# Kernel optimization log

Measured on AMD Instinct MI355X. Metric: run time of the kernel, lower is better.

## Reference

```python
import jax, jax.numpy as jnp
import numpy as np

H = 100      # STATE_SIZE
ATT = 100    # ATTENTION_SIZE
E = 32       # EMBEDDINGS_SIZE
V = 50257    # char vocab
TV = 60      # tag vocab
N = 2048     # source length (incl EOS padding)
T = 2048     # target length (incl EOS padding)
TT = 64      # number of tags


def lstm_cell(x, h, c, Wih, Whh, b):
    # torch gate order: i, f, g, o
    z = x @ Wih.T + h @ Whh.T + b
    i, f, g, o = jnp.split(z, 4)
    c = jax.nn.sigmoid(f) * c + jax.nn.sigmoid(i) * jnp.tanh(g)
    h = jax.nn.sigmoid(o) * jnp.tanh(c)
    return h, c


def lstm_scan(xs, Wih, Whh, b):
    Hs = Whh.shape[1]
    def step(carry, x):
        h, c = lstm_cell(x, carry[0], carry[1], Wih, Whh, b)
        return (h, c), h
    init = (jnp.zeros(Hs, xs.dtype), jnp.zeros(Hs, xs.dtype))
    _, ys = jax.lax.scan(step, init, xs)
    return ys


def setup_inputs() -> dict:
    key = jax.random.key(0)
    ks = iter(jax.random.split(key, 40))
    def rn(shape, s=0.1):
        return jax.random.normal(next(ks), shape, jnp.float32) * s
    return {
        "src_ids": jax.random.randint(next(ks), (1, N), 0, V),
        "tag_ids": jax.random.randint(next(ks), (1, TT), 0, TV),
        "out_ids": jax.random.randint(next(ks), (1, T), 0, V),
        "weight": jnp.ones((), jnp.float32),
        "emb_char": rn((V, E)),
        "emb_tag": rn((TV, E)),
        "enc_f_Wih": rn((4 * H, E)), "enc_f_Whh": rn((4 * H, H)), "enc_f_b": rn((4 * H,)),
        "enc_b_Wih": rn((4 * H, E)), "enc_b_Whh": rn((4 * H, H)), "enc_b_b": rn((4 * H,)),
        "tag_Wih": rn((4 * H, E)), "tag_Whh": rn((4 * H, H)), "tag_b": rn((4 * H,)),
        "dec_Wih": rn((4 * H, 3 * H + E)), "dec_Whh": rn((4 * H, H)), "dec_b": rn((4 * H,)),
        "attn_w1": rn((ATT, 2 * H)), "attn_w2": rn((ATT, 2 * H)), "attn_w3": rn((ATT, 5)),
        "attn_v": rn((1, ATT)),
        "tag_attn_w1": rn((ATT, H)), "tag_attn_w2": rn((ATT, 2 * H)), "tag_attn_v": rn((1, ATT)),
        "out_W": rn((V, H)), "out_b": rn((V,)),
    }


def reference(src_ids, tag_ids, out_ids, weight, emb_char, emb_tag,
              enc_f_Wih, enc_f_Whh, enc_f_b, enc_b_Wih, enc_b_Whh, enc_b_b,
              tag_Wih, tag_Whh, tag_b, dec_Wih, dec_Whh, dec_b,
              attn_w1, attn_w2, attn_w3, attn_v,
              tag_attn_w1, tag_attn_w2, tag_attn_v, out_W, out_b):
    x = emb_char[src_ids[0]]                       # (N, E)
    tg = emb_tag[tag_ids[0]]                       # (TT, E)
    # bidirectional char encoder
    yf = lstm_scan(x, enc_f_Wih, enc_f_Whh, enc_f_b)
    yb = lstm_scan(x[::-1], enc_b_Wih, enc_b_Whh, enc_b_b)[::-1]
    enc = jnp.concatenate([yf, yb], -1)            # (N, 2H)
    # tag encoder + self-attention residual (matches self_encode_tags)
    tv = lstm_scan(tg, tag_Wih, tag_Whh, tag_b)    # (TT, H)
    sa = jax.nn.softmax(tv @ tv.T, axis=-1)
    tagv = tv + jnp.einsum('sh,st->th', tv, sa)    # (TT, H)
    w1dt = enc @ attn_w1.T                         # (N, ATT)
    tag_w1dt = tagv @ tag_attn_w1.T                # (TT, ATT)
    eos_emb = emb_char[0]
    # initial decoder step on (enc_last, tag_last, eos_emb) with zero state
    x0 = jnp.concatenate([enc[-1], tagv[-1], eos_emb])
    h0, c0 = lstm_cell(x0, jnp.zeros(H, jnp.float32), jnp.zeros(H, jnp.float32),
                       dec_Wih, dec_Whh, dec_b)
    # teacher forcing: previous output embedding (EOS=id 0 at t=0)
    prev_ids = jnp.concatenate([jnp.zeros((1,), out_ids.dtype), out_ids[0, :-1]])
    prev_emb = emb_char[prev_ids]                  # (T, E)

    def step(carry, inp):
        h, c, prev_att = carry
        pe, oid = inp
        state = jnp.concatenate([h, c])            # (2H,)
        # tag attention
        taw = jax.nn.softmax(jnp.tanh(tag_w1dt + state @ tag_attn_w2.T) @ tag_attn_v[0])
        tag_ctx = taw @ tagv                       # (H,)
        new_state = state + jnp.concatenate([tag_ctx, tag_ctx])
        # char attention with 5-wide previous-attention feature
        scores = jnp.tanh(w1dt + new_state @ attn_w2.T + prev_att @ attn_w3.T) @ attn_v[0]
        aw = jax.nn.softmax(scores)                # (N,)
        ctx = aw @ enc                             # (2H,)
        startt = jnp.clip(jnp.argmax(aw) - 1, 0, N - 6)
        new_prev = jax.lax.dynamic_slice(aw, (startt,), (5,))
        hn, cn = lstm_cell(jnp.concatenate([ctx, tag_ctx, pe]), h, c,
                           dec_Wih, dec_Whh, dec_b)
        logits = hn @ out_W.T + out_b              # (V,)
        lt = -jax.nn.log_softmax(logits)[oid]
        return (hn, cn, new_prev), lt

    _, losses = jax.lax.scan(step, (h0, c0, jnp.zeros(5, jnp.float32)),
                             (prev_emb, out_ids[0]))
    return jnp.sum(losses) * weight
```

## Files before the change

kernel.cpp:

```cpp
#include <hip/hip_runtime.h>
#include <math.h>

#define NN   2048
#define TLEN 2048
#define TTAG 64
#define VOC  50257
#define GW   32
#define CHK  64
#define RECU 80
static_assert(GW * CHK == NN, "chunking");

#define OFF_XF    0
#define OFF_XB    (OFF_XF  + NN*400)
#define OFF_TGX   (OFF_XB  + NN*400)
#define OFF_PEW   (OFF_TGX + TTAG*400)
#define OFF_ENC   (OFF_PEW + TLEN*400)
#define OFF_W1DT  (OFF_ENC + NN*200)
#define OFF_TAGV  (OFF_W1DT+ NN*100)
#define OFF_TGW1  (OFF_TAGV+ TTAG*100)
#define OFF_TGW   (OFF_TGW1+ TTAG*100)
#define OFF_HOUT  (OFF_TGW + TTAG*400)
#define OFF_REC   (OFF_HOUT+ TLEN*100)
#define OFF_HC    (OFF_REC + 2*GW*RECU*2)
#define OFF_FLG   (OFF_HC  + 2*128*2)
#define OFF_PB    (OFF_FLG + 4096)


__device__ __forceinline__ float rcpf(float x){ return __builtin_amdgcn_rcpf(x); }
__device__ __forceinline__ float sigf(float x){ return rcpf(1.0f+__expf(-x)); }
__device__ __forceinline__ float tanhfast(float x){
  float e = __expf(2.0f*x);
  return 1.0f - 2.0f*rcpf(e+1.0f);
}
__device__ __forceinline__ unsigned short f2b(float x){
  unsigned b=__float_as_uint(x);
  return (unsigned short)((b + 0x7fffu + ((b>>16)&1u))>>16);
}
__device__ __forceinline__ unsigned pk2(float a,float b){ return (unsigned)f2b(a) | ((unsigned)f2b(b)<<16); }
__device__ __forceinline__ float blo(unsigned u){ return __uint_as_float(u<<16); }
__device__ __forceinline__ float bhi(unsigned u){ return __uint_as_float(u&0xffff0000u); }

__device__ __forceinline__ unsigned long long ald64(const unsigned long long* p){
  return __hip_atomic_load(p,__ATOMIC_RELAXED,__HIP_MEMORY_SCOPE_SYSTEM);
}
__device__ __forceinline__ void ast64(unsigned long long* p, unsigned long long v){
  __hip_atomic_store(p,v,__ATOMIC_RELAXED,__HIP_MEMORY_SCOPE_SYSTEM);
}
__device__ __forceinline__ void vm0(){ asm volatile("s_waitcnt vmcnt(0)" ::: "memory"); }

__global__ void kInit(float* ws){
  unsigned long long* f = (unsigned long long*)(ws + OFF_FLG);
  int i = blockIdx.x*256 + threadIdx.x;
  if (i < 2048) ast64(f+i, 0ull);
}

__global__ __launch_bounds__(512) void kPrep(
    const int* src, const int* tag, const int* oid,
    const float* emb_char, const float* emb_tag,
    const float* fWih, const float* fb,
    const float* bWih, const float* bb,
    const float* tWih, const float* tb,
    const float* dWih, const float* db, float* ws)
{
  int r = blockIdx.x, j = threadIdx.x;
  if (j >= 400) return;
  if (r < NN) {
    const float* e = emb_char + (size_t)src[r]*32;
    const float* Wr = fWih + j*32;
    float a = fb[j];
    #pragma unroll
    for (int q=0;q<32;q++) a += e[q]*Wr[q];
    ws[OFF_XF + r*400 + j] = a;
  } else if (r < 2*NN) {
    int n = r - NN;
    const float* e = emb_char + (size_t)src[n]*32;
    const float* Wr = bWih + j*32;
    float a = bb[j];
    #pragma unroll
    for (int q=0;q<32;q++) a += e[q]*Wr[q];
    ws[OFF_XB + n*400 + j] = a;
  } else if (r < 2*NN + TTAG) {
    int s = r - 2*NN;
    const float* e = emb_tag + (size_t)tag[s]*32;
    const float* Wr = tWih + j*32;
    float a = tb[j];
    #pragma unroll
    for (int q=0;q<32;q++) a += e[q]*Wr[q];
    ws[OFF_TGX + s*400 + j] = a;
  } else {
    int t = r - (2*NN + TTAG);
    int pid = (t==0) ? 0 : oid[t-1];
    const float* e = emb_char + (size_t)pid*32;
    const float* Wr = dWih + (size_t)j*332 + 300;
    float a = db[j];
    #pragma unroll
    for (int q=0;q<32;q++) a += e[q]*Wr[q];
    ws[OFF_PEW + t*400 + j] = a;
  }
}

struct EncShared {
  float tvs[TTAG*100];
  float sa [TTAG*64];
  float hbuf[100];
  float zbuf[400];
};

__device__ void lstm_block(const float* Whh, const float* xbase, float* ws,
                           int reverse, int col, EncShared* sh)
{
  int tid = threadIdx.x;
  float whh[100];
  if (tid < 400){
    #pragma unroll
    for (int k=0;k<100;k++) whh[k] = Whh[tid*100+k];
  }
  float c = 0.f;
  if (tid < 100) sh->hbuf[tid] = 0.f;
  __syncthreads();
  for (int i=0;i<NN;i++){
    int n = reverse ? (NN-1-i) : i;
    if (tid < 400){
      float z = xbase[n*400+tid];
      #pragma unroll
      for (int k=0;k<100;k++) z += whh[k]*sh->hbuf[k];
      sh->zbuf[tid] = z;
    }
    __syncthreads();
    if (tid < 100){
      float zi=sh->zbuf[tid], zf=sh->zbuf[tid+100], zg=sh->zbuf[tid+200], zo=sh->zbuf[tid+300];
      c = sigf(zf)*c + sigf(zi)*tanhfast(zg);
      float h = sigf(zo)*tanhfast(c);
      sh->hbuf[tid] = h;
      ws[OFF_ENC + n*200 + col + tid] = h;
    }
    __syncthreads();
  }
}

__global__ __launch_bounds__(512,1) void kEnc(
    const float* fWhh, const float* bWhh, const float* tWhh,
    const float* taw1, const float* dWih, float* ws)
{
  __shared__ EncShared sh;
  int b = blockIdx.x, tid = threadIdx.x;
  if (b == 0){ lstm_block(fWhh, ws+OFF_XF, ws, 0, 0,   &sh); return; }
  if (b == 1){ lstm_block(bWhh, ws+OFF_XB, ws, 1, 100, &sh); return; }

  {
    float whh[100];
    if (tid<400){
      #pragma unroll
      for (int k=0;k<100;k++) whh[k] = tWhh[tid*100+k];
    }
    float c = 0.f;
    if (tid<100) sh.hbuf[tid] = 0.f;
    __syncthreads();
    for (int s=0;s<TTAG;s++){
      if (tid<400){
        float z = ws[OFF_TGX + s*400 + tid];
        #pragma unroll
        for (int k=0;k<100;k++) z += whh[k]*sh.hbuf[k];
        sh.zbuf[tid] = z;
      }
      __syncthreads();
      if (tid<100){
        float zi=sh.zbuf[tid], zf=sh.zbuf[tid+100], zg=sh.zbuf[tid+200], zo=sh.zbuf[tid+300];
        c = sigf(zf)*c + sigf(zi)*tanhfast(zg);
        float h = sigf(zo)*tanhfast(c);
        sh.hbuf[tid] = h;
        sh.tvs[s*100+tid] = h;
      }
      __syncthreads();
    }
  }
  for (int idx=tid; idx<TTAG*TTAG; idx+=512){
    int s=idx>>6, t2=idx&63;
    float a=0.f;
    #pragma unroll 10
    for (int h=0;h<100;h++) a += sh.tvs[s*100+h]*sh.tvs[t2*100+h];
    sh.sa[idx]=a;
  }
  __syncthreads();
  if (tid<TTAG){
    float m=-1e30f;
    for (int t2=0;t2<64;t2++) m = fmaxf(m, sh.sa[tid*64+t2]);
    float sum=0.f;
    for (int t2=0;t2<64;t2++){ float e=__expf(sh.sa[tid*64+t2]-m); sh.sa[tid*64+t2]=e; sum+=e; }
    float r=1.f/sum;
    for (int t2=0;t2<64;t2++) sh.sa[tid*64+t2]*=r;
  }
  __syncthreads();
  float tvloc[13]; int cnt=0;
  for (int idx=tid; idx<TTAG*100; idx+=512){
    int t2=idx/100, hh=idx%100;
    float a = sh.tvs[t2*100+hh];
    for (int s=0;s<64;s++) a += sh.tvs[s*100+hh]*sh.sa[s*64+t2];
    tvloc[cnt++]=a;
    ws[OFF_TAGV+idx]=a;
  }
  __syncthreads();
  float* tagvs = sh.sa;
  cnt=0;
  for (int idx=tid; idx<TTAG*100; idx+=512) tagvs[idx]=tvloc[cnt++];
  __syncthreads();
  for (int idx=tid; idx<TTAG*100; idx+=512){
    int s=idx/100, k=idx%100;
    float a=0.f;
    #pragma unroll 10
    for (int h=0;h<100;h++) a += tagvs[s*100+h]*taw1[k*100+h];
    ws[OFF_TGW1+idx]=a;
  }
  for (int idx=tid; idx<TTAG*400; idx+=512){
    int s=idx/400, j=idx%400;
    const float* Wr = dWih + (size_t)j*332 + 200;
    float a=0.f;
    #pragma unroll 10
    for (int h=0;h<100;h++) a += tagvs[s*100+h]*Wr[h];
    ws[OFF_TGW+idx]=a;
  }
}

__global__ void kMid(const float* aw1, float* ws){
  __shared__ float er[200];
  int n=blockIdx.x, tid=threadIdx.x;
  for (int i=tid;i<200;i+=128) er[i]=ws[OFF_ENC+n*200+i];
  __syncthreads();
  if (tid<100){
    const float* Wr = aw1 + tid*200;
    float a=0.f;
    #pragma unroll 8
    for (int d=0;d<200;d++) a += er[d]*Wr[d];
    ws[OFF_W1DT + n*100 + tid]=a;
  }
}

__global__ __launch_bounds__(512) void kDec(
    const float* dWhh, const float* dWih,
    const float* aw2, const float* aw3, const float* av,
    const float* taw2, const float* tav, float* ws)
{
  __shared__ unsigned aw2L[100*101];
  __shared__ unsigned tw2L[100*101];
  __shared__ unsigned tw1L[TTAG*51];
  __shared__ unsigned tagvL[TTAG*51];
  __shared__ unsigned w1L[CHK*51];
  __shared__ unsigned encL[CHK*101];
  __shared__ float tavL[100], avL[100], aw3L[500];
  __shared__ float hL[100], cL[100], tcL[100], tsaL[100], nsL[200];
  __shared__ float uL[TTAG], tawL[TTAG];
  __shared__ float ctxL[200], a23L[100], ctxpL[200];
  __shared__ float srowL[CHK], eRL[CHK];
  __shared__ float zOwnL[16];
  __shared__ float prevL[5];
  __shared__ float Sg;
  __shared__ int   amiL;

  const int tid = threadIdx.x;
  const int w   = blockIdx.x;
  unsigned long long* REC = (unsigned long long*)(ws + OFF_REC);
  unsigned long long* HC  = (unsigned long long*)(ws + OFF_HC);
  unsigned long long* FLG = (unsigned long long*)(ws + OFF_FLG);

  const int nu = (w<4)? 4 : 3;
  const int u0 = (w<4)? w*4 : 16 + (w-4)*3;
  const int nact = nu*4;
  const int jslot = tid>>5, l = tid&31;

  unsigned wca0=0,wca1=0,wca2=0,wca3=0, wha0=0,wha1=0, wta0=0,wta1=0;
  int row=0;
  if (jslot < nact){
    row = (jslot&3)*100 + u0 + (jslot>>2);
    const float* Wr = dWih + (size_t)row*332;
    wca0=pk2(Wr[2*l],Wr[2*l+1]);
    wca1=pk2(Wr[2*(32+l)],Wr[2*(32+l)+1]);
    wca2=pk2(Wr[2*(64+l)],Wr[2*(64+l)+1]);
    if (l<4) wca3=pk2(Wr[2*(96+l)],Wr[2*(96+l)+1]);
    const float* Wh = dWhh + (size_t)row*100;
    wha0=pk2(Wh[2*l],Wh[2*l+1]);
    if (l<18) wha1=pk2(Wh[2*(32+l)],Wh[2*(32+l)+1]);
    const float* Wt = Wr + 200;
    wta0=pk2(Wt[2*l],Wt[2*l+1]);
    if (l<18) wta1=pk2(Wt[2*(32+l)],Wt[2*(32+l)+1]);
  }
  for (int i=tid;i<100*100;i+=512){ int k=i/100,p=i%100; aw2L[k*101+p]=pk2(aw2 [k*200+2*p], aw2 [k*200+2*p+1]); }
  for (int i=tid;i<100*100;i+=512){ int k=i/100,p=i%100; tw2L[k*101+p]=pk2(taw2[k*200+2*p], taw2[k*200+2*p+1]); }
  for (int i=tid;i<TTAG*50;i+=512){ int s=i/50,p=i%50; tw1L[s*51+p]=pk2(ws[OFF_TGW1+s*100+2*p], ws[OFF_TGW1+s*100+2*p+1]); }
  for (int i=tid;i<TTAG*50;i+=512){ int s=i/50,p=i%50; tagvL[s*51+p]=pk2(ws[OFF_TAGV+s*100+2*p], ws[OFF_TAGV+s*100+2*p+1]); }
  for (int i=tid;i<CHK*50;i+=512){ int r=i/50,p=i%50; w1L[r*51+p]=pk2(ws[OFF_W1DT+(w*CHK+r)*100+2*p], ws[OFF_W1DT+(w*CHK+r)*100+2*p+1]); }
  for (int i=tid;i<CHK*100;i+=512){ int r=i/100,p=i%100; encL[r*101+p]=pk2(ws[OFF_ENC+(w*CHK+r)*200+2*p], ws[OFF_ENC+(w*CHK+r)*200+2*p+1]); }
  if (tid<100){ tavL[tid]=tav[tid]; avL[tid]=av[tid]; }
  for (int i=tid;i<500;i+=512) aw3L[i]=aw3[i];
  if (tid<5)   prevL[tid]=0.f;
  if (tid<200) ctxL[tid]=ws[OFF_ENC + 2047*200 + tid];
  __syncthreads();

  if (jslot < nact){
    float acc=0.f;
    { unsigned u=wca0; acc += ctxL[2*l]*blo(u) + ctxL[2*l+1]*bhi(u); }
    { unsigned u=wca1; acc += ctxL[2*(32+l)]*blo(u) + ctxL[2*(32+l)+1]*bhi(u); }
    { unsigned u=wca2; acc += ctxL[2*(64+l)]*blo(u) + ctxL[2*(64+l)+1]*bhi(u); }
    if (l<4){ unsigned u=wca3; acc += ctxL[2*(96+l)]*blo(u) + ctxL[2*(96+l)+1]*bhi(u); }
    acc += __shfl_xor(acc,1,32); acc += __shfl_xor(acc,2,32);
    acc += __shfl_xor(acc,4,32); acc += __shfl_xor(acc,8,32); acc += __shfl_xor(acc,16,32);
    if (l==0) zOwnL[jslot] = acc + ws[OFF_TGW + 63*400 + row] + ws[OFF_PEW + row];
  }
  __syncthreads();
  float cOwn = 0.f;
  if (tid < nu){
    float zi=zOwnL[tid*4+0], zg=zOwnL[tid*4+2], zo=zOwnL[tid*4+3];
    float cc = sigf(zi)*tanhfast(zg);
    float hh = sigf(zo)*tanhfast(cc);
    cOwn = cc;
    ast64(HC + 128 + (u0+tid), (unsigned long long)pk2(hh,cc) | (1ull<<32));
  }

  for (int t=0; t<TLEN; ++t){
    const unsigned sq = (unsigned)(t+1);
    unsigned long long* slot = REC + (size_t)(t&1)*GW*RECU;
    unsigned long long* hcg  = HC + (size_t)((t+1)&1)*128;
    unsigned long long* hcp  = HC + (size_t)(t&1)*128;
    unsigned long long* fr   = FLG + (size_t)(t&1)*GW*16;
    unsigned long long* fh   = FLG + (size_t)(64 + (t&1)*GW)*16;

    if (tid < 100){
      const unsigned long long* p0 = hcg + tid;
      unsigned long long v;
      for(;;){ v=ald64(p0); if((unsigned)(v>>32)==sq) break; __builtin_amdgcn_s_sleep(1); }
      unsigned lo=(unsigned)v;
      hL[tid]=blo(lo); cL[tid]=bhi(lo);
    }
    __syncthreads();
    if (tid<400){
      int k=tid>>2, q=tid&3, off=q*50;
      const float* sb = (off<100)? (hL+off) : (cL+(off-100));
      float acc=0.f;
      #pragma unroll
      for (int i=0;i<25;i++){ unsigned u=tw2L[k*101+q*25+i]; acc += sb[2*i]*blo(u) + sb[2*i+1]*bhi(u); }
      acc += __shfl_xor(acc,1,4); acc += __shfl_xor(acc,2,4);
      if (q==0) tsaL[k]=acc;
    }
    __syncthreads();
    {
      int sp=tid>>3, l8=tid&7;
      float acc=0.f;
      for (int k=l8;k<100;k+=8){
        unsigned u=tw1L[sp*51+(k>>1)];
        float w1v=(k&1)? bhi(u) : blo(u);
        acc += tanhfast(w1v + tsaL[k]) * tavL[k];
      }
      acc += __shfl_xor(acc,1,8); acc += __shfl_xor(acc,2,8); acc += __shfl_xor(acc,4,8);
      if (l8==0) uL[sp]=acc;
    }
    __syncthreads();
    if (tid<64){
      float v=uL[tid], m=v;
      for (int d=1;d<64;d<<=1) m=fmaxf(m,__shfl_xor(m,d,64));
      float e=__expf(v-m), ssum=e;
      for (int d=1;d<64;d<<=1) ssum+=__shfl_xor(ssum,d,64);
      tawL[tid]=e*rcpf(ssum);
    }
    __syncthreads();
    if (tid<400){
      int hh=tid>>2, q=tid&3;
      float acc=0.f;
      #pragma unroll
      for (int i=0;i<16;i++){
        int s=q*16+i;
        unsigned u=tagvL[s*51+(hh>>1)];
        acc += tawL[s]*((hh&1)? bhi(u):blo(u));
      }
      acc += __shfl_xor(acc,1,4); acc += __shfl_xor(acc,2,4);
      if (q==0){ tcL[hh]=acc; nsL[hh]=hL[hh]+acc; nsL[100+hh]=cL[hh]+acc; }
    }
    __syncthreads();
    if (tid<400){
      int k=tid>>2, q=tid&3, off=q*50;
      float acc=0.f;
      #pragma unroll
      for (int i=0;i<25;i++){ unsigned u=aw2L[k*101+q*25+i]; acc += nsL[off+2*i]*blo(u) + nsL[off+2*i+1]*bhi(u); }
      acc += __shfl_xor(acc,1,4); acc += __shfl_xor(acc,2,4);
      if (q==0){
        float a3=0.f;
        #pragma unroll
        for (int i=0;i<5;i++) a3 += prevL[i]*aw3L[k*5+i];
        a23L[k]=acc+a3;
      }
    }
    __syncthreads();
    {
      int r=tid>>3, l8=tid&7;
      float acc=0.f;
      for (int k=l8;k<100;k+=8){
        unsigned u=w1L[r*51+(k>>1)];
        float w1v=(k&1)? bhi(u) : blo(u);
        acc += tanhfast(w1v + a23L[k]) * avL[k];
      }
      acc += __shfl_xor(acc,1,8); acc += __shfl_xor(acc,2,8); acc += __shfl_xor(acc,4,8);
      if (l8==0){ srowL[r]=acc; eRL[r]=__expf(acc); }
    }
    __syncthreads();
    if (tid<400){
      int d=tid>>1, hf=tid&1;
      float acc=0.f;
      #pragma unroll 8
      for (int i=0;i<32;i++){
        int rr=hf*32+i;
        unsigned u=encL[rr*101+(d>>1)];
        acc += eRL[rr]*((d&1)? bhi(u):blo(u));
      }
      acc += __shfl_xor(acc,1,2);
      if (hf==0) ctxpL[d]=acc;
    } else if (tid>=448){
      int lane = tid-448;
      float eS = eRL[lane];
      float sv = srowL[lane]; int si = w*CHK+lane;
      #pragma unroll
      for (int d=1;d<64;d<<=1){
        eS += __shfl_xor(eS,d,64);
        float ov=__shfl_xor(sv,d,64); int oi=__shfl_xor(si,d,64);
        if (ov>sv || (ov==sv && oi<si)){ sv=ov; si=oi; }
      }
      unsigned long long* rp = slot + (size_t)w*RECU;
      if (lane < 16){ int j=lane;
        ast64(rp+50+j, (unsigned long long)pk2(srowL[4*j],srowL[4*j+1])
                     | ((unsigned long long)pk2(srowL[4*j+2],srowL[4*j+3])<<32));
      } else if (lane==16)
        ast64(rp+66, (unsigned long long)__float_as_uint(eS)
                   | ((unsigned long long)__float_as_uint(sv)<<32));
      else if (lane==17)
        ast64(rp+67, (unsigned long long)__float_as_uint(sv)
                   | ((unsigned long long)(unsigned)si<<32));
      vm0();
      if (lane==0) ast64(fh + (size_t)w*16, (unsigned long long)sq);
    }
    __syncthreads();

    #define ZPRE_ROW() do{ \
      if (jslot < nact){ \
        float acc=0.f; \
        { unsigned u=wha0; acc += hL[2*l]*blo(u) + hL[2*l+1]*bhi(u); } \
        if (l<18){ unsigned u=wha1; acc += hL[2*(32+l)]*blo(u) + hL[2*(32+l)+1]*bhi(u); } \
        { unsigned u=wta0; acc += tcL[2*l]*blo(u) + tcL[2*l+1]*bhi(u); } \
        if (l<18){ unsigned u=wta1; acc += tcL[2*(32+l)]*blo(u) + tcL[2*(32+l)+1]*bhi(u); } \
        acc += __shfl_xor(acc,1,32); acc += __shfl_xor(acc,2,32); \
        acc += __shfl_xor(acc,4,32); acc += __shfl_xor(acc,8,32); acc += __shfl_xor(acc,16,32); \
        if (l==0) zOwnL[jslot] = acc + ws[OFF_PEW + t*400 + row]; \
      } \
    }while(0)

    if (tid < 448){
      ZPRE_ROW();
      if (tid < 64){
        int ok = (tid >= GW) ? 1 : 0;
        for(;;){
          if (!ok) ok = ((unsigned)ald64(fr + (size_t)tid*16) == sq);
          if (__all(ok)) break;
        }
      }
    } else {
      int lane = tid-448;
      unsigned long long* rp = slot + (size_t)w*RECU;
      if (lane < 50)
        ast64(rp+lane, (unsigned long long)pk2(ctxpL[4*lane],ctxpL[4*lane+1])
                     | ((unsigned long long)pk2(ctxpL[4*lane+2],ctxpL[4*lane+3])<<32));
      vm0();
      if (lane==0) ast64(fr + (size_t)w*16, (unsigned long long)sq);
      ZPRE_ROW();
      {
        int r = lane&31, up = lane>>5;
        const unsigned long long* fp = fh + (size_t)r*16;
        for(;;){ if ((unsigned)ald64(fp)==sq) break; __builtin_amdgcn_s_sleep(1); }
        unsigned long long v = ald64(slot + (size_t)r*RECU + 66 + up);
        if (!up){
          float ss = __uint_as_float((unsigned)v);
          #pragma unroll
          for (int d=1;d<32;d<<=1) ss += __shfl_xor(ss,d,32);
          if (r==0) Sg = ss;
        } else {
          float pv = __uint_as_float((unsigned)v);
          int   pi = (int)(unsigned)(v>>32);
          #pragma unroll
          for (int d=1;d<32;d<<=1){
            float ov=__shfl_xor(pv,d,32); int oi=__shfl_xor(pi,d,32);
            if (ov>pv || (ov==pv && oi<pi)){ pv=ov; pi=oi; }
          }
          if (r==0) amiL = pi;
        }
      }
    }
    __syncthreads();
    if (tid<400){
      float rS = rcpf(Sg);
      int dw=tid>>3, s8=tid&7;
      float c0=0.f,c1=0.f,c2=0.f,c3=0.f;
      #pragma unroll
      for (int i=0;i<4;i++){
        unsigned long long p = ald64(slot + (size_t)(s8*4+i)*RECU + dw);
        unsigned lo=(unsigned)p, hi=(unsigned)(p>>32);
        c0 += blo(lo); c1 += bhi(lo);
        c2 += blo(hi); c3 += bhi(hi);
      }
      #pragma unroll
      for (int d=1;d<8;d<<=1){
        c0 += __shfl_xor(c0,d,8); c1 += __shfl_xor(c1,d,8);
        c2 += __shfl_xor(c2,d,8); c3 += __shfl_xor(c3,d,8);
      }
      if (s8==0){
        ctxL[4*dw+0]=c0*rS; ctxL[4*dw+1]=c1*rS;
        ctxL[4*dw+2]=c2*rS; ctxL[4*dw+3]=c3*rS;
      }
    }
    __syncthreads();
    if (jslot < nact){
      float acc=0.f;
      { unsigned u=wca0; acc += ctxL[2*l]*blo(u) + ctxL[2*l+1]*bhi(u); }
      { unsigned u=wca1; acc += ctxL[2*(32+l)]*blo(u) + ctxL[2*(32+l)+1]*bhi(u); }
      { unsigned u=wca2; acc += ctxL[2*(64+l)]*blo(u) + ctxL[2*(64+l)+1]*bhi(u); }
      if (l<4){ unsigned u=wca3; acc += ctxL[2*(96+l)]*blo(u) + ctxL[2*(96+l)+1]*bhi(u); }
      acc += __shfl_xor(acc,1,32); acc += __shfl_xor(acc,2,32);
      acc += __shfl_xor(acc,4,32); acc += __shfl_xor(acc,8,32); acc += __shfl_xor(acc,16,32);
      if (l==0) zOwnL[jslot] += acc;
    }
    __syncthreads();
    if (tid>=440 && tid<445){
      int i=tid-440;
      int st = amiL-1; st = st<0?0:st; st = st>NN-6?NN-6:st;
      int g = st+i, r=g>>6, lr=g&63;
      unsigned long long v = ald64(slot + (size_t)r*RECU + 50 + (lr>>2));
      unsigned half = (lr&2)? (unsigned)(v>>32) : (unsigned)v;
      float sc = (lr&1)? bhi(half) : blo(half);
      prevL[i] = __expf(sc) * rcpf(Sg);
    }
    if (tid < nu){
      float zi=zOwnL[tid*4+0], zf=zOwnL[tid*4+1], zg=zOwnL[tid*4+2], zo=zOwnL[tid*4+3];
      float cc = sigf(zf)*cOwn + sigf(zi)*tanhfast(zg);
      float hh = sigf(zo)*tanhfast(cc);
      cOwn = cc;
      ast64(hcp + (u0+tid), (unsigned long long)pk2(hh,cc)
                          | ((unsigned long long)(sq+1)<<32));
      ws[OFF_HOUT + t*100 + (u0+tid)] = hh;
    }
  }
}

__global__ __launch_bounds__(256) void kLoss(const float* outW, const float* outb,
                                             const int* oid, float* ws)
{
  const int b=blockIdx.x, tid=threadIdx.x;
  const int tile=b>>1, hf=b&1, t0=tile*16;
  __shared__ float s_hn[16*100];
  __shared__ int   s_oid[16];
  __shared__ float red[4][16][3];
  for (int i=tid;i<1600;i+=256) s_hn[i]=ws[OFF_HOUT + t0*100 + i];
  if (tid<16) s_oid[tid]=oid[t0+tid];
  __syncthreads();
  const int VSPLIT = 25129;
  int vbeg = hf? VSPLIT : 0;
  int vend = hf? VOC : VSPLIT;
  float rm[16], rs[16], ol[16];
  #pragma unroll
  for (int tt=0;tt<16;tt++){ rm[tt]=-1e30f; rs[tt]=0.f; ol[tt]=-1e30f; }
  for (int v=vbeg+tid; v<vend; v+=256){
    const float4* wr = (const float4*)(outW + (size_t)v*100);
    float acc[16];
    #pragma unroll
    for (int tt=0;tt<16;tt++) acc[tt]=0.f;
    #pragma unroll 5
    for (int q=0;q<25;q++){
      float4 wv = wr[q];
      #pragma unroll
      for (int tt=0;tt<16;tt++){
        float4 hv = *(const float4*)(s_hn + tt*100 + q*4);
        acc[tt] += wv.x*hv.x + wv.y*hv.y + wv.z*hv.z + wv.w*hv.w;
      }
    }
    float bb = outb[v];
    #pragma unroll
    for (int tt=0;tt<16;tt++){
      float lg = acc[tt] + bb;
      if (v == s_oid[tt]) ol[tt] = fmaxf(ol[tt], lg);
      if (lg <= rm[tt]) rs[tt] += __expf(lg - rm[tt]);
      else { rs[tt] = rs[tt]*__expf(rm[tt]-lg) + 1.0f; rm[tt]=lg; }
    }
  }
  int wv2=tid>>6, ln=tid&63;
  #pragma unroll
  for (int tt=0;tt<16;tt++){
    float m=rm[tt], sv=rs[tt], o=ol[tt];
    for (int d=1;d<64;d<<=1){
      float om=__shfl_xor(m,d,64), os=__shfl_xor(sv,d,64), oo=__shfl_xor(o,d,64);
      float M2=fmaxf(m,om);
      sv = sv*__expf(m-M2) + os*__expf(om-M2);
      m=M2; o=fmaxf(o,oo);
    }
    if (ln==0){ red[wv2][tt][0]=m; red[wv2][tt][1]=sv; red[wv2][tt][2]=o; }
  }
  __syncthreads();
  if (tid<16){
    float M=-1e30f;
    for (int q=0;q<4;q++) M=fmaxf(M,red[q][tid][0]);
    float S=0.f, O=-1e30f;
    for (int q=0;q<4;q++){ S += red[q][tid][1]*__expf(red[q][tid][0]-M); O=fmaxf(O,red[q][tid][2]); }
    float* pb = ws + OFF_PB + (((tile*2)+hf)*16 + tid)*4;
    pb[0]=M; pb[1]=S; pb[2]=O;
  }
}

__global__ void kFinal(const float* weight, float* ws, float* out){
  __shared__ float red[256];
  int tid=threadIdx.x;
  float acc=0.f;
  for (int t=tid;t<TLEN;t+=256){
    int tile=t>>4, tt=t&15;
    const float* p0 = ws + OFF_PB + ((tile*2+0)*16+tt)*4;
    const float* p1 = ws + OFF_PB + ((tile*2+1)*16+tt)*4;
    float M=fmaxf(p0[0],p1[0]);
    float S=p0[1]*__expf(p0[0]-M) + p1[1]*__expf(p1[0]-M);
    float O=fmaxf(p0[2],p1[2]);
    acc += (M + logf(S)) - O;
  }
  red[tid]=acc; __syncthreads();
  for (int d=128; d>0; d>>=1){
    if (tid<d) red[tid]+=red[tid+d];
    __syncthreads();
  }
  if (tid==0) out[0]=red[0]*weight[0];
}

extern "C" void kernel_launch(void* const* d_in, const int* in_sizes, int n_in,
                              void* d_out, int out_size, void* d_ws, size_t ws_size,
                              hipStream_t stream) {
  const int*   src      = (const int*)  d_in[0];
  const int*   tag      = (const int*)  d_in[1];
  const int*   oid      = (const int*)  d_in[2];
  const float* weight   = (const float*)d_in[3];
  const float* emb_char = (const float*)d_in[4];
  const float* emb_tag  = (const float*)d_in[5];
  const float* fWih=(const float*)d_in[6],  *fWhh=(const float*)d_in[7],  *fb=(const float*)d_in[8];
  const float* bWih=(const float*)d_in[9],  *bWhh=(const float*)d_in[10], *bb=(const float*)d_in[11];
  const float* tWih=(const float*)d_in[12], *tWhh=(const float*)d_in[13], *tb=(const float*)d_in[14];
  const float* dWih=(const float*)d_in[15], *dWhh=(const float*)d_in[16], *db=(const float*)d_in[17];
  const float* aw1 =(const float*)d_in[18], *aw2=(const float*)d_in[19];
  const float* aw3 =(const float*)d_in[20], *av =(const float*)d_in[21];
  const float* taw1=(const float*)d_in[22], *taw2=(const float*)d_in[23], *tavv=(const float*)d_in[24];
  const float* outW=(const float*)d_in[25], *outb=(const float*)d_in[26];
  float* ws  = (float*)d_ws;
  float* out = (float*)d_out;

  kInit<<<8, 256, 0, stream>>>(ws);
  kPrep<<<2*NN+TTAG+TLEN, 512, 0, stream>>>(src,tag,oid,emb_char,emb_tag,
                                            fWih,fb,bWih,bb,tWih,tb,dWih,db,ws);
  kEnc<<<3,512,0,stream>>>(fWhh,bWhh,tWhh,taw1,dWih,ws);
  kMid<<<NN,128,0,stream>>>(aw1,ws);
  kDec<<<GW,512,0,stream>>>(dWhh,dWih,aw2,aw3,av,taw2,tavv,ws);
  kLoss<<<256,256,0,stream>>>(outW,outb,oid,ws);
  kFinal<<<1,256,0,stream>>>(weight,ws,out);
}
```

Measured before the change: 24.94 ms.

## Map LSTM gate rows to wavefronts and drop per-step block barriers

Reassigns decoder LSTM gate rows so each hidden unit's four gates sit in one 64-lane wavefront (16 lanes per gate). The gate nonlinearity can then run on shuffled values without shared-memory staging and its extra __syncthreads. The tag-attention softmax drops its max-subtraction pass and barrier: it stores exp(score) directly and normalises by a sum computed alongside the context dot product. The h/tag-context part of the gate pre-activation is kept in a register across the spin-wait instead of written to shared memory. Skipping the max subtraction risks overflow if tag scores get large, and fewer lanes per gate row means more serial FMAs per lane.

Result: slower. 25.88 ms (+3.8%).

```diff
diff --git a/kernel.cpp b/kernel.cpp
--- a/kernel.cpp
+++ b/kernel.cpp
@@ -248,10 +248,9 @@
   __shared__ unsigned encL[CHK*101];
   __shared__ float tavL[100], avL[100], aw3L[500];
   __shared__ float hL[100], cL[100], tcL[100], tsaL[100], nsL[200];
-  __shared__ float uL[TTAG], tawL[TTAG];
+  __shared__ float uL[TTAG];
   __shared__ float ctxL[200], a23L[100], ctxpL[200];
   __shared__ float srowL[CHK], eRL[CHK];
-  __shared__ float zOwnL[16];
   __shared__ float prevL[5];
   __shared__ float Sg;
   __shared__ int   amiL;
@@ -264,24 +263,25 @@
 
   const int nu = (w<4)? 4 : 3;
   const int u0 = (w<4)? w*4 : 16 + (w-4)*3;
-  const int nact = nu*4;
-  const int jslot = tid>>5, l = tid&31;
-
-  unsigned wca0=0,wca1=0,wca2=0,wca3=0, wha0=0,wha1=0, wta0=0,wta1=0;
+  const int uu  = tid>>6;
+  const int g16 = (tid>>4)&3;
+  const int l16 = tid&15;
+  const int l64 = tid&63;
+  const int uact = (uu < nu);
+
+  unsigned wca[7]={0,0,0,0,0,0,0}, wha[4]={0,0,0,0}, wta[4]={0,0,0,0};
   int row=0;
-  if (jslot < nact){
-    row = (jslot&3)*100 + u0 + (jslot>>2);
+  if (uact){
+    row = g16*100 + u0 + uu;
     const float* Wr = dWih + (size_t)row*332;
-    wca0=pk2(Wr[2*l],Wr[2*l+1]);
-    wca1=pk2(Wr[2*(32+l)],Wr[2*(32+l)+1]);
-    wca2=pk2(Wr[2*(64+l)],Wr[2*(64+l)+1]);
-    if (l<4) wca3=pk2(Wr[2*(96+l)],Wr[2*(96+l)+1]);
+    #pragma unroll
+    for (int i=0;i<7;i++){ int p=l16+16*i; if (p<100) wca[i]=pk2(Wr[2*p],Wr[2*p+1]); }
     const float* Wh = dWhh + (size_t)row*100;
-    wha0=pk2(Wh[2*l],Wh[2*l+1]);
-    if (l<18) wha1=pk2(Wh[2*(32+l)],Wh[2*(32+l)+1]);
+    #pragma unroll
+    for (int i=0;i<4;i++){ int p=l16+16*i; if (p<50) wha[i]=pk2(Wh[2*p],Wh[2*p+1]); }
     const float* Wt = Wr + 200;
-    wta0=pk2(Wt[2*l],Wt[2*l+1]);
-    if (l<18) wta1=pk2(Wt[2*(32+l)],Wt[2*(32+l)+1]);
+    #pragma unroll
+    for (int i=0;i<4;i++){ int p=l16+16*i; if (p<50) wta[i]=pk2(Wt[2*p],Wt[2*p+1]); }
   }
   for (int i=tid;i<100*100;i+=512){ int k=i/100,p=i%100; aw2L[k*101+p]=pk2(aw2 [k*200+2*p], aw2 [k*200+2*p+1]); }
   for (int i=tid;i<100*100;i+=512){ int k=i/100,p=i%100; tw2L[k*101+p]=pk2(taw2[k*200+2*p], taw2[k*200+2*p+1]); }
@@ -295,24 +295,22 @@
   if (tid<200) ctxL[tid]=ws[OFF_ENC + 2047*200 + tid];
   __syncthreads();
 
-  if (jslot < nact){
+  float cOwn = 0.f;
+  if (uact){
     float acc=0.f;
-    { unsigned u=wca0; acc += ctxL[2*l]*blo(u) + ctxL[2*l+1]*bhi(u); }
-    { unsigned u=wca1; acc += ctxL[2*(32+l)]*blo(u) + ctxL[2*(32+l)+1]*bhi(u); }
-    { unsigned u=wca2; acc += ctxL[2*(64+l)]*blo(u) + ctxL[2*(64+l)+1]*bhi(u); }
-    if (l<4){ unsigned u=wca3; acc += ctxL[2*(96+l)]*blo(u) + ctxL[2*(96+l)+1]*bhi(u); }
-    acc += __shfl_xor(acc,1,32); acc += __shfl_xor(acc,2,32);
-    acc += __shfl_xor(acc,4,32); acc += __shfl_xor(acc,8,32); acc += __shfl_xor(acc,16,32);
-    if (l==0) zOwnL[jslot] = acc + ws[OFF_TGW + 63*400 + row] + ws[OFF_PEW + row];
-  }
-  __syncthreads();
-  float cOwn = 0.f;
-  if (tid < nu){
-    float zi=zOwnL[tid*4+0], zg=zOwnL[tid*4+2], zo=zOwnL[tid*4+3];
-    float cc = sigf(zi)*tanhfast(zg);
-    float hh = sigf(zo)*tanhfast(cc);
-    cOwn = cc;
-    ast64(HC + 128 + (u0+tid), (unsigned long long)pk2(hh,cc) | (1ull<<32));
+    #pragma unroll
+    for (int i=0;i<7;i++){ int p=l16+16*i; if (p<100){ unsigned u=wca[i]; acc += ctxL[2*p]*blo(u) + ctxL[2*p+1]*bhi(u); } }
+    #pragma unroll
+    for (int d=1;d<16;d<<=1) acc += __shfl_xor(acc,d,16);
+    float v = acc;
+    if (l16==0) v += ws[OFF_TGW + 63*400 + row] + ws[OFF_PEW + row];
+    float zi=__shfl(v,0,64), zg=__shfl(v,32,64), zo=__shfl(v,48,64);
+    if (l64==0){
+      float cc = sigf(zi)*tanhfast(zg);
+      float hh = sigf(zo)*tanhfast(cc);
+      cOwn = cc;
+      ast64(HC + 128 + (u0+uu), (unsigned long long)pk2(hh,cc) | (1ull<<32));
+    }
   }
 
   for (int t=0; t<TLEN; ++t){
@@ -350,28 +348,26 @@
         acc += tanhfast(w1v + tsaL[k]) * tavL[k];
       }
       acc += __shfl_xor(acc,1,8); acc += __shfl_xor(acc,2,8); acc += __shfl_xor(acc,4,8);
-      if (l8==0) uL[sp]=acc;
-    }
-    __syncthreads();
-    if (tid<64){
-      float v=uL[tid], m=v;
-      for (int d=1;d<64;d<<=1) m=fmaxf(m,__shfl_xor(m,d,64));
-      float e=__expf(v-m), ssum=e;
-      for (int d=1;d<64;d<<=1) ssum+=__shfl_xor(ssum,d,64);
-      tawL[tid]=e*rcpf(ssum);
+      if (l8==0) uL[sp]=__expf(acc);
     }
     __syncthreads();
     if (tid<400){
       int hh=tid>>2, q=tid&3;
-      float acc=0.f;
+      float acc=0.f, accE=0.f;
       #pragma unroll
       for (int i=0;i<16;i++){
         int s=q*16+i;
+        float e=uL[s];
         unsigned u=tagvL[s*51+(hh>>1)];
-        acc += tawL[s]*((hh&1)? bhi(u):blo(u));
-      }
-      acc += __shfl_xor(acc,1,4); acc += __shfl_xor(acc,2,4);
-      if (q==0){ tcL[hh]=acc; nsL[hh]=hL[hh]+acc; nsL[100+hh]=cL[hh]+acc; }
+        acc += e*((hh&1)? bhi(u):blo(u));
+        accE += e;
+      }
+      acc  += __shfl_xor(acc,1,4);  acc  += __shfl_xor(acc,2,4);
+      accE += __shfl_xor(accE,1,4); accE += __shfl_xor(accE,2,4);
+      if (q==0){
+        float tc = acc * rcpf(accE);
+        tcL[hh]=tc; nsL[hh]=hL[hh]+tc; nsL[100+hh]=cL[hh]+tc;
+      }
     }
     __syncthreads();
     if (tid<400){
@@ -436,21 +432,18 @@
     }
     __syncthreads();
 
-    #define ZPRE_ROW() do{ \
-      if (jslot < nact){ \
-        float acc=0.f; \
-        { unsigned u=wha0; acc += hL[2*l]*blo(u) + hL[2*l+1]*bhi(u); } \
-        if (l<18){ unsigned u=wha1; acc += hL[2*(32+l)]*blo(u) + hL[2*(32+l)+1]*bhi(u); } \
-        { unsigned u=wta0; acc += tcL[2*l]*blo(u) + tcL[2*l+1]*bhi(u); } \
-        if (l<18){ unsigned u=wta1; acc += tcL[2*(32+l)]*blo(u) + tcL[2*(32+l)+1]*bhi(u); } \
-        acc += __shfl_xor(acc,1,32); acc += __shfl_xor(acc,2,32); \
-        acc += __shfl_xor(acc,4,32); acc += __shfl_xor(acc,8,32); acc += __shfl_xor(acc,16,32); \
-        if (l==0) zOwnL[jslot] = acc + ws[OFF_PEW + t*400 + row]; \
-      } \
-    }while(0)
-
+    float zacc = 0.f;
     if (tid < 448){
-      ZPRE_ROW();
+      if (uact){
+        #pragma unroll
+        for (int i=0;i<4;i++){
+          int p=l16+16*i;
+          if (p<50){
+            unsigned u=wha[i]; zacc += hL[2*p]*blo(u) + hL[2*p+1]*bhi(u);
+            unsigned u2=wta[i]; zacc += tcL[2*p]*blo(u2) + tcL[2*p+1]*bhi(u2);
+          }
+        }
+      }
       if (tid < 64){
         int ok = (tid >= GW) ? 1 : 0;
         for(;;){
@@ -466,7 +459,6 @@
                      | ((unsigned long long)pk2(ctxpL[4*lane+2],ctxpL[4*lane+3])<<32));
       vm0();
       if (lane==0) ast64(fr + (size_t)w*16, (unsigned long long)sq);
-      ZPRE_ROW();
       {
         int r = lane&31, up = lane>>5;
         const unsigned long long* fp = fh + (size_t)r*16;
@@ -512,17 +504,24 @@
       }
     }
     __syncthreads();
-    if (jslot < nact){
-      float acc=0.f;
-      { unsigned u=wca0; acc += ctxL[2*l]*blo(u) + ctxL[2*l+1]*bhi(u); }
-      { unsigned u=wca1; acc += ctxL[2*(32+l)]*blo(u) + ctxL[2*(32+l)+1]*bhi(u); }
-      { unsigned u=wca2; acc += ctxL[2*(64+l)]*blo(u) + ctxL[2*(64+l)+1]*bhi(u); }
-      if (l<4){ unsigned u=wca3; acc += ctxL[2*(96+l)]*blo(u) + ctxL[2*(96+l)+1]*bhi(u); }
-      acc += __shfl_xor(acc,1,32); acc += __shfl_xor(acc,2,32);
-      acc += __shfl_xor(acc,4,32); acc += __shfl_xor(acc,8,32); acc += __shfl_xor(acc,16,32);
-      if (l==0) zOwnL[jslot] += acc;
-    }
-    __syncthreads();
+    if (uact){
+      float acc = zacc;
+      #pragma unroll
+      for (int i=0;i<7;i++){ int p=l16+16*i; if (p<100){ unsigned u=wca[i]; acc += ctxL[2*p]*blo(u) + ctxL[2*p+1]*bhi(u); } }
+      #pragma unroll
+      for (int d=1;d<16;d<<=1) acc += __shfl_xor(acc,d,16);
+      float v = acc;
+      if (l16==0) v += ws[OFF_PEW + t*400 + row];
+      float zi=__shfl(v,0,64), zf=__shfl(v,16,64), zg=__shfl(v,32,64), zo=__shfl(v,48,64);
+      if (l64==0){
+        float cc = sigf(zf)*cOwn + sigf(zi)*tanhfast(zg);
+        float hh = sigf(zo)*tanhfast(cc);
+        cOwn = cc;
+        ast64(hcp + (u0+uu), (unsigned long long)pk2(hh,cc)
+                           | ((unsigned long long)(sq+1)<<32));
+        ws[OFF_HOUT + t*100 + (u0+uu)] = hh;
+      }
+    }
     if (tid>=440 && tid<445){
       int i=tid-440;
       int st = amiL-1; st = st<0?0:st; st = st>NN-6?NN-6:st;
@@ -531,15 +530,6 @@
       unsigned half = (lr&2)? (unsigned)(v>>32) : (unsigned)v;
       float sc = (lr&1)? bhi(half) : blo(half);
       prevL[i] = __expf(sc) * rcpf(Sg);
-    }
-    if (tid < nu){
-      float zi=zOwnL[tid*4+0], zf=zOwnL[tid*4+1], zg=zOwnL[tid*4+2], zo=zOwnL[tid*4+3];
-      float cc = sigf(zf)*cOwn + sigf(zi)*tanhfast(zg);
-      float hh = sigf(zo)*tanhfast(cc);
-      cOwn = cc;
-      ast64(hcp + (u0+tid), (unsigned long long)pk2(hh,cc)
-                          | ((unsigned long long)(sq+1)<<32));
-      ws[OFF_HOUT + t*100 + (u0+tid)] = hh;
     }
   }
 }
```
